# Kernel tuning notes

Hardware: AMD Instinct MI355X
Metric: run time of the kernel (lower is better)

## Reference

```python
import jax, jax.numpy as jnp
import numpy as np

EPS = 0.01

def setup_inputs() -> dict:
    key = jax.random.key(0)
    k1, k2, k3 = jax.random.split(key, 3)
    B, H, S = 2, 16, 2048
    x = jax.random.normal(k1, (B, H, S, S), dtype=jnp.float32)
    bias_p = jax.random.uniform(k2, (H, 1, 1), dtype=jnp.float32) * 2.0
    bias_a = jax.random.uniform(k3, (H, 1, 1), dtype=jnp.float32) * 1.0
    return {"x": x, "bias_p": bias_p, "bias_a": bias_a}

def reference(x, bias_p, bias_a):
    sk = x.shape[-1]
    # diff[i, j] = i - j on the lower triangle (incl. diagonal), 0 above it
    idx = jnp.arange(sk)
    diff = jnp.tril(idx[:, None] - idx[None, :]).astype(x.dtype)  # [sk, sk]
    p = jnp.maximum(bias_p, EPS)  # [H, 1, 1]
    a = jnp.maximum(bias_a, EPS)  # [H, 1, 1]
    bias = -p * jnp.log1p(a * diff)  # [H, sk, sk]
    return x + bias  # broadcast over batch
```

## Files before the change

kernel.cpp:

```cpp
#include <hip/hip_runtime.h>


#define EPS 0.01f
#define LN2 0.69314718055994530942f

__global__ __launch_bounds__(256) void ParallelKerpleLog_50216757625001_kernel(
    const float4* __restrict__ x,
    const float* __restrict__ bias_p,
    const float* __restrict__ bias_a,
    float4* __restrict__ out,
    int n4)
{
    __shared__ float sc[16];
    __shared__ float sa[16];
    const int t = threadIdx.x;
    if (t < 16) {
        float p = fmaxf(bias_p[t], EPS);
        float a = fmaxf(bias_a[t], EPS);
        sc[t] = -p * LN2;
        sa[t] = a;
    }
    __syncthreads();

    const int stride = gridDim.x * blockDim.x;
    for (int idx = blockIdx.x * blockDim.x + t; idx < n4; idx += stride) {
        const int e = idx << 2;
        const int j = e & 2047;
        const int i = (e >> 11) & 2047;
        const int h = (e >> 22) & 15;
        const float c = sc[h];
        const float a = sa[h];

        const float4 v = x[idx];
        const int d0 = i - j;
        float r[4];
        const float vv[4] = {v.x, v.y, v.z, v.w};
        #pragma unroll
        for (int k = 0; k < 4; ++k) {
            int d = d0 - k;
            d = d > 0 ? d : 0;
            const float tt = fmaf(a, (float)d, 1.0f);
            const float l = __log2f(tt);
            r[k] = fmaf(c, l, vv[k]);
        }
        out[idx] = make_float4(r[0], r[1], r[2], r[3]);
    }
}

extern "C" void kernel_launch(void* const* d_in, const int* in_sizes, int n_in,
                              void* d_out, int out_size, void* d_ws, size_t ws_size,
                              hipStream_t stream) {
    const float4* x      = (const float4*)d_in[0];
    const float*  bias_p = (const float*)d_in[1];
    const float*  bias_a = (const float*)d_in[2];
    float* out = (float*)d_out;

    const int n4 = out_size >> 2;
    const int threads = 256;
    const int blocks = 2048;

    ParallelKerpleLog_50216757625001_kernel<<<blocks, threads, 0, stream>>>(
        x, bias_p, bias_a, (float4*)out, n4);
}
```

Measured before the change: 221.5 us.

## Assign fixed per-head chunks to blocks with batched nontemporal loads and stores

Replaces the grid-stride loop with a fixed mapping: each block handles a contiguous 16K-float4 chunk belonging to a single head, so the head's bias constants are computed once per block without shared memory or a barrier. Each thread issues eight independent nontemporal vector loads before computing and storing, which raises memory-level parallelism and bypasses cache retention for streaming data. The mapping hardcodes the tensor shape and assumes an exact grid of 2048 blocks, so it no longer has a bounds check.

```diff
diff --git a/kernel.cpp b/kernel.cpp
--- a/kernel.cpp
+++ b/kernel.cpp
@@ -4,61 +4,60 @@
 #define EPS 0.01f
 #define LN2 0.69314718055994530942f
 
+typedef float f32x4 __attribute__((ext_vector_type(4)));
+
 __global__ __launch_bounds__(256) void ParallelKerpleLog_50216757625001_kernel(
-    const float4* __restrict__ x,
+    const f32x4* __restrict__ x,
     const float* __restrict__ bias_p,
     const float* __restrict__ bias_a,
-    float4* __restrict__ out,
-    int n4)
+    f32x4* __restrict__ out)
 {
-    __shared__ float sc[16];
-    __shared__ float sa[16];
-    const int t = threadIdx.x;
-    if (t < 16) {
-        float p = fmaxf(bias_p[t], EPS);
-        float a = fmaxf(bias_a[t], EPS);
-        sc[t] = -p * LN2;
-        sa[t] = a;
-    }
-    __syncthreads();
+    const int bid = blockIdx.x;
+    const int h   = (bid >> 6) & 15;
+    const float a = fmaxf(bias_a[h], EPS);
+    const float c = -fmaxf(bias_p[h], EPS) * LN2;
 
-    const int stride = gridDim.x * blockDim.x;
-    for (int idx = blockIdx.x * blockDim.x + t; idx < n4; idx += stride) {
-        const int e = idx << 2;
-        const int j = e & 2047;
-        const int i = (e >> 11) & 2047;
-        const int h = (e >> 22) & 15;
-        const float c = sc[h];
-        const float a = sa[h];
+    const int base4 = ((bid >> 6) << 20) + ((bid & 63) << 14);
+    const int idx0  = base4 + threadIdx.x;
 
-        const float4 v = x[idx];
-        const int d0 = i - j;
-        float r[4];
-        const float vv[4] = {v.x, v.y, v.z, v.w};
+    #pragma unroll
+    for (int it = 0; it < 8; ++it) {
+        int   id[8];
+        f32x4 v[8];
         #pragma unroll
-        for (int k = 0; k < 4; ++k) {
-            int d = d0 - k;
-            d = d > 0 ? d : 0;
-            const float tt = fmaf(a, (float)d, 1.0f);
-            const float l = __log2f(tt);
-            r[k] = fmaf(c, l, vv[k]);
+        for (int k = 0; k < 8; ++k) {
+            id[k] = idx0 + (it * 8 + k) * 256;
+            v[k]  = __builtin_nontemporal_load(&x[id[k]]);
         }
-        out[idx] = make_float4(r[0], r[1], r[2], r[3]);
+        f32x4 r[8];
+        #pragma unroll
+        for (int k = 0; k < 8; ++k) {
+            const int e  = id[k] << 2;
+            const int j  = e & 2047;
+            const int i  = (e >> 11) & 2047;
+            const int d0 = i - j;
+            #pragma unroll
+            for (int q = 0; q < 4; ++q) {
+                int d = d0 - q;
+                d = d > 0 ? d : 0;
+                r[k][q] = fmaf(c, __log2f(fmaf(a, (float)d, 1.0f)), v[k][q]);
+            }
+        }
+        #pragma unroll
+        for (int k = 0; k < 8; ++k) {
+            __builtin_nontemporal_store(r[k], &out[id[k]]);
+        }
     }
 }
 
 extern "C" void kernel_launch(void* const* d_in, const int* in_sizes, int n_in,
                               void* d_out, int out_size, void* d_ws, size_t ws_size,
                               hipStream_t stream) {
-    const float4* x      = (const float4*)d_in[0];
+    const f32x4* x       = (const f32x4*)d_in[0];
     const float*  bias_p = (const float*)d_in[1];
     const float*  bias_a = (const float*)d_in[2];
-    float* out = (float*)d_out;
+    f32x4* out = (f32x4*)d_out;
 
-    const int n4 = out_size >> 2;
-    const int threads = 256;
-    const int blocks = 2048;
-
-    ParallelKerpleLog_50216757625001_kernel<<<blocks, threads, 0, stream>>>(
-        x, bias_p, bias_a, (float4*)out, n4);
+    ParallelKerpleLog_50216757625001_kernel<<<2048, 256, 0, stream>>>(
+        x, bias_p, bias_a, out);
 }
```

New measurement: 197.2 us. -11.0%, faster.
